# Performance work log

Hardware: AMD Instinct MI355X
Metric: run time of the kernel (lower is better)

Reference implementation:

```python
import jax, jax.numpy as jnp
import numpy as np

N, T = 2000, 8
INFEAT, HID, OUT, H = 32, 16, 32, 4
ALPHA = 0.2
D1 = HID * H   # 64, layer-1 GRU dim (concat heads)
D2 = OUT       # 32, layer-2 GRU dim (mean heads)
NEG = -1e9


def setup_inputs() -> dict:
    key = jax.random.key(0)
    ks = jax.random.split(key, 12)
    xav = lambda k, shape, fi, fo: (jax.random.normal(k, shape, dtype=jnp.float32)
                                    * np.float32(np.sqrt(2.0 / (fi + fo))))
    # sparse-ish binary adjacency with self loops, per timestep
    A = (jax.random.uniform(ks[0], (T, N, N)) < 0.01).astype(jnp.float32)
    A = jnp.maximum(A, jnp.eye(N, dtype=jnp.float32)[None])
    feats = jax.random.normal(ks[1], (T, N, INFEAT), dtype=jnp.float32) * 0.1
    return {
        "A": A,
        "feats": feats,
        "gat1_W": xav(ks[2], (H, INFEAT, HID), INFEAT, HID),
        "gat1_a": xav(ks[3], (H, 2, HID), 2 * HID, 1),
        "gru1_W": xav(ks[4], (3, N, D1, D1), D1, D1),
        "gru1_U": xav(ks[5], (3, N, D1, D1), D1, D1),
        "gru1_b": jnp.zeros((3, N, D1), jnp.float32),
        "q1": xav(ks[6], (N, D1), N, D1),   # GAT_init_features, layer 1
        "gat2_W": xav(ks[7], (H, D1, OUT), D1, OUT),
        "gat2_a": xav(ks[8], (H, 2, OUT), 2 * OUT, 1),
        "gru2_W": xav(ks[9], (3, N, D2, D2), D2, D2),
        "gru2_U": xav(ks[10], (3, N, D2, D2), D2, D2),
        "gru2_b": jnp.zeros((3, N, D2), jnp.float32),
        "q2": xav(ks[11], (N, D2), N, D2),  # GAT_init_features, layer 2
    }


def _gat(x, At, W, a, concat):
    # x: [N,F], At: [N,N], W: [H,F,D], a: [H,2,D]
    h = jnp.einsum('nf,hfd->hnd', x, W)                       # [H,N,D]
    e_src = jnp.einsum('hnd,hd->hn', h, a[:, 0])              # [H,N]
    e_dst = jnp.einsum('hnd,hd->hn', h, a[:, 1])
    e = jax.nn.leaky_relu(e_src[:, :, None] + e_dst[:, None, :], ALPHA)
    e = jnp.where(At[None] > 0, e, NEG)
    att = jax.nn.softmax(e, axis=-1)                          # [H,N,N]
    o = jnp.einsum('hnm,hmd->hnd', att, h)
    if concat:
        return jax.nn.elu(o).transpose(1, 0, 2).reshape(x.shape[0], -1)  # [N,H*D]
    return o.mean(axis=0)                                     # [N,D]


def _gru_step(Q, Z, Wg, Ug, bg):
    # batched per-node mat_GRU_cell: Wg/Ug [3,N,D,D], bg [3,N,D]; gates: update, reset, htilda
    wz = jnp.einsum('gnij,nj->gni', Wg, Z) + bg               # [3,N,D]
    upd = jax.nn.sigmoid(wz[0] + jnp.einsum('nij,nj->ni', Ug[0], Q))
    rst = jax.nn.sigmoid(wz[1] + jnp.einsum('nij,nj->ni', Ug[1], Q))
    hcap = jnp.tanh(wz[2] + jnp.einsum('nij,nj->ni', Ug[2], rst * Q))
    return (1.0 - upd) * Q + upd * hcap


def _grcu_layer(A, feats, q0, W, a, Wg, Ug, bg, concat):
    def step(Q, inp):
        At, xt = inp
        Z = _gat(xt, At, W, a, concat)
        Qn = _gru_step(Q, Z, Wg, Ug, bg)
        return Qn, Qn
    _, seq = jax.lax.scan(step, q0, (A, feats))
    return seq  # [T,N,Dim]


def reference(A, feats, gat1_W, gat1_a, gru1_W, gru1_U, gru1_b, q1,
              gat2_W, gat2_a, gru2_W, gru2_U, gru2_b, q2):
    s1 = _grcu_layer(A, feats, q1, gat1_W, gat1_a, gru1_W, gru1_U, gru1_b, True)
    s2 = _grcu_layer(A, s1, q2, gat2_W, gat2_a, gru2_W, gru2_U, gru2_b, False)
    return s2.reshape(-1, s2.shape[-1])  # torch.cat(out_seq, dim=0) -> [T*N, OUT]
```

## Files before the change

kernel.cpp:

```cpp
#include <hip/hip_runtime.h>
#include <cstdint>
#include <cstddef>

#define NNODES 2000
#define TSTEPS 8
#define NHEADS 4
#define CAP    96
#define NROWS  (TSTEPS * NNODES)

__global__ void k1_csr_gath1(const float* __restrict__ A,
                             int* __restrict__ nbr, int* __restrict__ cnt,
                             const float* __restrict__ feats,
                             const float* __restrict__ W, const float* __restrict__ a,
                             float* __restrict__ hbuf, float* __restrict__ es,
                             float* __restrict__ ed) {
    const int lane = threadIdx.x;
    if (blockIdx.x < NROWS) {
        const int row = blockIdx.x;
        const float4* Ar4 = reinterpret_cast<const float4*>(A + (size_t)row * NNODES);
        int* outp = nbr + (size_t)row * CAP;
        const unsigned long long lmask = (1ull << lane) - 1ull;
        int c = 0;
        for (int j4 = lane; j4 < NNODES / 4; j4 += 64) {
            float4 v = Ar4[j4];
            #pragma unroll
            for (int cc = 0; cc < 4; ++cc) {
                float x = (cc == 0) ? v.x : (cc == 1) ? v.y : (cc == 2) ? v.z : v.w;
                bool p = x > 0.0f;
                unsigned long long m = __ballot(p);
                int off = __popcll(m & lmask);
                if (p && c + off < CAP) outp[c + off] = j4 * 4 + cc;
                c += (int)__popcll(m);
            }
        }
        if (lane == 0) cnt[row] = (c > CAP ? CAP : c);
    } else {
        const int b = blockIdx.x - NROWS;
        const int t = b / NNODES, n = b % NNODES;
        constexpr int F = 32, D = 16;
        const int h = lane / D, d = lane % D;
        const float* xr = feats + (size_t)b * F;
        const float* Wp = W + (size_t)h * F * D + d;
        float acc = 0.f;
        #pragma unroll
        for (int f = 0; f < F; ++f) acc += xr[f] * Wp[f * D];
        hbuf[(((size_t)t * NHEADS + h) * NNODES + n) * D + d] = acc;
        float s0 = acc * a[(h * 2 + 0) * D + d];
        float s1 = acc * a[(h * 2 + 1) * D + d];
        #pragma unroll
        for (int s = D / 2; s > 0; s >>= 1) {
            s0 += __shfl_down(s0, s, D);
            s1 += __shfl_down(s1, s, D);
        }
        if (d == 0) {
            es[((size_t)t * NHEADS + h) * NNODES + n] = s0;
            ed[((size_t)t * NHEADS + h) * NNODES + n] = s1;
        }
    }
}

template<int D, bool CONCAT>
__global__ void gat_attn_all_kernel(const int* __restrict__ nbr, const int* __restrict__ cnt_arr,
                                    const float* __restrict__ hbuf, const float* __restrict__ es,
                                    const float* __restrict__ ed, float* __restrict__ Z) {
    const int b = blockIdx.x;
    const int t = b / NNODES, n = b % NNODES;
    const int tid = threadIdx.x;
    const int h = tid / D, d = tid % D;
    const int cnt = cnt_arr[b];
    const int* idx = nbr + (size_t)b * CAP;
    const float* esb = es + (size_t)t * NHEADS * NNODES;
    const float* edb = ed + (size_t)t * NHEADS * NNODES;
    const float* hb  = hbuf + (size_t)t * NHEADS * NNODES * D;
    __shared__ int mlist[CAP];
    __shared__ float eds[NHEADS][CAP];
    for (int k = tid; k < cnt; k += NHEADS * D) mlist[k] = idx[k];
    __syncthreads();
    for (int k = d; k < cnt; k += D) eds[h][k] = edb[(size_t)h * NNODES + mlist[k]];
    __syncthreads();
    const float esv = esb[(size_t)h * NNODES + n];
    float maxv = -1e30f;
    for (int k = 0; k < cnt; ++k) {
        float v = esv + eds[h][k];
        v = v > 0.f ? v : 0.2f * v;
        maxv = fmaxf(maxv, v);
    }
    float wsum = 0.f, acc = 0.f;
    for (int k = 0; k < cnt; ++k) {
        float v = esv + eds[h][k];
        v = v > 0.f ? v : 0.2f * v;
        float w = __expf(v - maxv);
        wsum += w;
        acc += w * hb[((size_t)h * NNODES + mlist[k]) * D + d];
    }
    float o = acc / wsum;
    if constexpr (CONCAT) {
        float e = o > 0.f ? o : (__expf(o) - 1.0f);
        Z[(size_t)b * (NHEADS * D) + h * D + d] = e;
    } else {
        __shared__ float red[NHEADS][D];
        red[h][d] = o;
        __syncthreads();
        if (h == 0) Z[(size_t)b * D + d] =
            (red[0][d] + red[1][d] + red[2][d] + red[3][d]) * 0.25f;
    }
}

__global__ __launch_bounds__(256, 1)
void wzgru1_gath2_kernel(const float* __restrict__ Wg, const float* __restrict__ Ug,
                         const float* __restrict__ bg, const float* __restrict__ Z,
                         const float* __restrict__ q0,
                         const float* __restrict__ W2, const float* __restrict__ a2,
                         float* __restrict__ h2, float* __restrict__ es2,
                         float* __restrict__ ed2) {
    constexpr int D = 64;
    constexpr int QUADS = 4;
    constexpr int TPB = 256;
    constexpr int F4R = D / 4;
    const int n = blockIdx.x, tid = threadIdx.x;
    const int quad = tid & (QUADS - 1);
    const int row  = tid / QUADS;
    const int cbase = quad * 16;
    __shared__ float Zs[TSTEPS][D];
    __shared__ float Qh[TSTEPS][D];
    __shared__ float Qs[D], rq[D];

    for (int idx = tid; idx < TSTEPS * F4R; idx += TPB) {
        int t = idx / F4R, i4 = idx % F4R;
        reinterpret_cast<float4*>(&Zs[t][0])[i4] =
            reinterpret_cast<const float4*>(Z + ((size_t)t * NNODES + n) * D)[i4];
    }
    if (tid < D) Qs[tid] = q0[(size_t)n * D + tid];
    float bgv[3];
    #pragma unroll
    for (int g = 0; g < 3; ++g) bgv[g] = bg[((size_t)g * NNODES + n) * D + row];

    float wseg[3][16], useg[3][16];
    #pragma unroll
    for (int g = 0; g < 3; ++g) {
        const float4* W4 = reinterpret_cast<const float4*>(
            Wg + ((size_t)g * NNODES + n) * D * D + (size_t)row * D + cbase);
        #pragma unroll
        for (int c = 0; c < 4; ++c) {
            float4 v = W4[c];
            wseg[g][c * 4 + 0] = v.x; wseg[g][c * 4 + 1] = v.y;
            wseg[g][c * 4 + 2] = v.z; wseg[g][c * 4 + 3] = v.w;
        }
    }
    #pragma unroll
    for (int g = 0; g < 3; ++g) {
        const float4* U4 = reinterpret_cast<const float4*>(
            Ug + ((size_t)g * NNODES + n) * D * D + (size_t)row * D + cbase);
        #pragma unroll
        for (int c = 0; c < 4; ++c) {
            float4 v = U4[c];
            useg[g][c * 4 + 0] = v.x; useg[g][c * 4 + 1] = v.y;
            useg[g][c * 4 + 2] = v.z; useg[g][c * 4 + 3] = v.w;
        }
    }
    __syncthreads();

    float wzr[3][TSTEPS];
    #pragma unroll
    for (int t = 0; t < TSTEPS; ++t) {
        float z16[16];
        #pragma unroll
        for (int c = 0; c < 4; ++c) {
            float4 v = reinterpret_cast<const float4*>(&Zs[t][cbase])[c];
            z16[c * 4 + 0] = v.x; z16[c * 4 + 1] = v.y;
            z16[c * 4 + 2] = v.z; z16[c * 4 + 3] = v.w;
        }
        #pragma unroll
        for (int g = 0; g < 3; ++g) {
            float p = 0.f;
            #pragma unroll
            for (int c = 0; c < 16; ++c) p += wseg[g][c] * z16[c];
            p += __shfl_xor(p, 1, 4); p += __shfl_xor(p, 2, 4);
            wzr[g][t] = p + bgv[g];
        }
    }

    #pragma unroll
    for (int t = 0; t < TSTEPS; ++t) {
        float q16[16];
        #pragma unroll
        for (int c = 0; c < 4; ++c) {
            float4 v = reinterpret_cast<const float4*>(&Qs[cbase])[c];
            q16[c * 4 + 0] = v.x; q16[c * 4 + 1] = v.y;
            q16[c * 4 + 2] = v.z; q16[c * 4 + 3] = v.w;
        }
        float p0 = 0.f, p1 = 0.f;
        #pragma unroll
        for (int c = 0; c < 16; ++c) { p0 += useg[0][c] * q16[c]; p1 += useg[1][c] * q16[c]; }
        p0 += __shfl_xor(p0, 1, 4); p0 += __shfl_xor(p0, 2, 4);
        p1 += __shfl_xor(p1, 1, 4); p1 += __shfl_xor(p1, 2, 4);
        const float qrow = Qs[row];
        const float zg = 1.f / (1.f + __expf(-(wzr[0][t] + p0)));
        const float rg = 1.f / (1.f + __expf(-(wzr[1][t] + p1)));
        if (quad == 0) rq[row] = rg * qrow;
        __syncthreads();
        float p2 = 0.f;
        {
            float r16[16];
            #pragma unroll
            for (int c = 0; c < 4; ++c) {
                float4 v = reinterpret_cast<const float4*>(&rq[cbase])[c];
                r16[c * 4 + 0] = v.x; r16[c * 4 + 1] = v.y;
                r16[c * 4 + 2] = v.z; r16[c * 4 + 3] = v.w;
            }
            #pragma unroll
            for (int c = 0; c < 16; ++c) p2 += useg[2][c] * r16[c];
        }
        p2 += __shfl_xor(p2, 1, 4); p2 += __shfl_xor(p2, 2, 4);
        const float hcap = tanhf(wzr[2][t] + p2);
        const float qn = (1.f - zg) * qrow + zg * hcap;
        if (quad == 0) {
            Qs[row] = qn;
            Qh[t][row] = qn;
        }
        __syncthreads();
    }

    const int lane = tid & 63;
    const int hh = tid >> 6;
    const int d2 = lane >> 1;
    const int fh = lane & 1;
    float w2seg[32];
    const float* W2p = W2 + ((size_t)hh * 64 + fh * 32) * 32 + d2;
    #pragma unroll
    for (int j = 0; j < 32; ++j) w2seg[j] = W2p[(size_t)j * 32];
    const float a0 = a2[(hh * 2 + 0) * 32 + d2];
    const float a1 = a2[(hh * 2 + 1) * 32 + d2];
    #pragma unroll
    for (int t = 0; t < TSTEPS; ++t) {
        float p = 0.f;
        #pragma unroll
        for (int j = 0; j < 32; ++j) p += w2seg[j] * Qh[t][fh * 32 + j];
        p += __shfl_xor(p, 1, 64);
        if (fh == 0) h2[(((size_t)t * NHEADS + hh) * NNODES + n) * 32 + d2] = p;
        float e0 = (fh == 0) ? p * a0 : 0.f;
        float e1 = (fh == 0) ? p * a1 : 0.f;
        #pragma unroll
        for (int s = 2; s <= 32; s <<= 1) {
            e0 += __shfl_xor(e0, s, 64);
            e1 += __shfl_xor(e1, s, 64);
        }
        if (lane == 0) {
            es2[((size_t)t * NHEADS + hh) * NNODES + n] = e0;
            ed2[((size_t)t * NHEADS + hh) * NNODES + n] = e1;
        }
    }
}

template<int D>
__global__ __launch_bounds__((D / 16) * D, 1)
void wzgru_kernel(const float* __restrict__ Wg, const float* __restrict__ Ug,
                  const float* __restrict__ bg, const float* __restrict__ Z,
                  const float* __restrict__ q0, float* __restrict__ outp) {
    constexpr int QUADS = D / 16;
    constexpr int TPB = QUADS * D;
    constexpr int F4R = D / 4;
    const int n = blockIdx.x, tid = threadIdx.x;
    const int quad = tid & (QUADS - 1);
    const int row  = tid / QUADS;
    const int cbase = quad * 16;
    __shared__ float Zs[TSTEPS][D];
    __shared__ float Qs[D], rq[D];

    for (int idx = tid; idx < TSTEPS * F4R; idx += TPB) {
        int t = idx / F4R, i4 = idx % F4R;
        reinterpret_cast<float4*>(&Zs[t][0])[i4] =
            reinterpret_cast<const float4*>(Z + ((size_t)t * NNODES + n) * D)[i4];
    }
    if (tid < D) Qs[tid] = q0[(size_t)n * D + tid];
    float bgv[3];
    #pragma unroll
    for (int g = 0; g < 3; ++g) bgv[g] = bg[((size_t)g * NNODES + n) * D + row];

    float wseg[3][16], useg[3][16];
    #pragma unroll
    for (int g = 0; g < 3; ++g) {
        const float4* W4 = reinterpret_cast<const float4*>(
            Wg + ((size_t)g * NNODES + n) * D * D + (size_t)row * D + cbase);
        #pragma unroll
        for (int c = 0; c < 4; ++c) {
            float4 v = W4[c];
            wseg[g][c * 4 + 0] = v.x; wseg[g][c * 4 + 1] = v.y;
            wseg[g][c * 4 + 2] = v.z; wseg[g][c * 4 + 3] = v.w;
        }
    }
    #pragma unroll
    for (int g = 0; g < 3; ++g) {
        const float4* U4 = reinterpret_cast<const float4*>(
            Ug + ((size_t)g * NNODES + n) * D * D + (size_t)row * D + cbase);
        #pragma unroll
        for (int c = 0; c < 4; ++c) {
            float4 v = U4[c];
            useg[g][c * 4 + 0] = v.x; useg[g][c * 4 + 1] = v.y;
            useg[g][c * 4 + 2] = v.z; useg[g][c * 4 + 3] = v.w;
        }
    }
    __syncthreads();

    float wzr[3][TSTEPS];
    #pragma unroll
    for (int t = 0; t < TSTEPS; ++t) {
        float z16[16];
        #pragma unroll
        for (int c = 0; c < 4; ++c) {
            float4 v = reinterpret_cast<const float4*>(&Zs[t][cbase])[c];
            z16[c * 4 + 0] = v.x; z16[c * 4 + 1] = v.y;
            z16[c * 4 + 2] = v.z; z16[c * 4 + 3] = v.w;
        }
        #pragma unroll
        for (int g = 0; g < 3; ++g) {
            float p = 0.f;
            #pragma unroll
            for (int c = 0; c < 16; ++c) p += wseg[g][c] * z16[c];
            if constexpr (QUADS == 4) { p += __shfl_xor(p, 1, 4); p += __shfl_xor(p, 2, 4); }
            else                      { p += __shfl_xor(p, 1, 2); }
            wzr[g][t] = p + bgv[g];
        }
    }

    #pragma unroll
    for (int t = 0; t < TSTEPS; ++t) {
        float q16[16];
        #pragma unroll
        for (int c = 0; c < 4; ++c) {
            float4 v = reinterpret_cast<const float4*>(&Qs[cbase])[c];
            q16[c * 4 + 0] = v.x; q16[c * 4 + 1] = v.y;
            q16[c * 4 + 2] = v.z; q16[c * 4 + 3] = v.w;
        }
        float p0 = 0.f, p1 = 0.f;
        #pragma unroll
        for (int c = 0; c < 16; ++c) { p0 += useg[0][c] * q16[c]; p1 += useg[1][c] * q16[c]; }
        if constexpr (QUADS == 4) {
            p0 += __shfl_xor(p0, 1, 4); p0 += __shfl_xor(p0, 2, 4);
            p1 += __shfl_xor(p1, 1, 4); p1 += __shfl_xor(p1, 2, 4);
        } else {
            p0 += __shfl_xor(p0, 1, 2); p1 += __shfl_xor(p1, 1, 2);
        }
        const float qrow = Qs[row];
        const float zg = 1.f / (1.f + __expf(-(wzr[0][t] + p0)));
        const float rg = 1.f / (1.f + __expf(-(wzr[1][t] + p1)));
        if (quad == 0) rq[row] = rg * qrow;
        __syncthreads();
        float p2 = 0.f;
        {
            float r16[16];
            #pragma unroll
            for (int c = 0; c < 4; ++c) {
                float4 v = reinterpret_cast<const float4*>(&rq[cbase])[c];
                r16[c * 4 + 0] = v.x; r16[c * 4 + 1] = v.y;
                r16[c * 4 + 2] = v.z; r16[c * 4 + 3] = v.w;
            }
            #pragma unroll
            for (int c = 0; c < 16; ++c) p2 += useg[2][c] * r16[c];
        }
        if constexpr (QUADS == 4) { p2 += __shfl_xor(p2, 1, 4); p2 += __shfl_xor(p2, 2, 4); }
        else                      { p2 += __shfl_xor(p2, 1, 2); }
        const float hcap = tanhf(wzr[2][t] + p2);
        const float qn = (1.f - zg) * qrow + zg * hcap;
        if (quad == 0) {
            Qs[row] = qn;
            outp[((size_t)t * NNODES + n) * D + row] = qn;
        }
        __syncthreads();
    }
}

extern "C" void kernel_launch(void* const* d_in, const int* in_sizes, int n_in,
                              void* d_out, int out_size, void* d_ws, size_t ws_size,
                              hipStream_t stream) {
    const float* A      = (const float*)d_in[0];
    const float* feats  = (const float*)d_in[1];
    const float* gat1_W = (const float*)d_in[2];
    const float* gat1_a = (const float*)d_in[3];
    const float* gru1_W = (const float*)d_in[4];
    const float* gru1_U = (const float*)d_in[5];
    const float* gru1_b = (const float*)d_in[6];
    const float* q1     = (const float*)d_in[7];
    const float* gat2_W = (const float*)d_in[8];
    const float* gat2_a = (const float*)d_in[9];
    const float* gru2_W = (const float*)d_in[10];
    const float* gru2_U = (const float*)d_in[11];
    const float* gru2_b = (const float*)d_in[12];
    const float* q2     = (const float*)d_in[13];
    float* out = (float*)d_out;

    char* ws = (char*)d_ws;
    int*   nbr  = (int*)ws;    ws += (size_t)NROWS * CAP * 4;
    int*   cnt  = (int*)ws;    ws += (size_t)NROWS * 4;
    float* h1   = (float*)ws;  ws += (size_t)TSTEPS * NHEADS * NNODES * 16 * 4;
    float* es1  = (float*)ws;  ws += (size_t)TSTEPS * NHEADS * NNODES * 4;
    float* ed1  = (float*)ws;  ws += (size_t)TSTEPS * NHEADS * NNODES * 4;
    float* Z1   = (float*)ws;  ws += (size_t)TSTEPS * NNODES * 64 * 4;
    float* h2   = (float*)ws;  ws += (size_t)TSTEPS * NHEADS * NNODES * 32 * 4;
    float* es2  = (float*)ws;  ws += (size_t)TSTEPS * NHEADS * NNODES * 4;
    float* ed2  = (float*)ws;  ws += (size_t)TSTEPS * NHEADS * NNODES * 4;
    float* Z2   = (float*)ws;  ws += (size_t)TSTEPS * NNODES * 32 * 4;

    k1_csr_gath1<<<2 * NROWS, 64, 0, stream>>>(A, nbr, cnt, feats, gat1_W, gat1_a,
                                               h1, es1, ed1);
    gat_attn_all_kernel<16, true><<<NROWS, 64, 0, stream>>>(nbr, cnt, h1, es1, ed1, Z1);
    wzgru1_gath2_kernel<<<NNODES, 256, 0, stream>>>(gru1_W, gru1_U, gru1_b, Z1, q1,
                                                    gat2_W, gat2_a, h2, es2, ed2);
    gat_attn_all_kernel<32, false><<<NROWS, 128, 0, stream>>>(nbr, cnt, h2, es2, ed2, Z2);
    wzgru_kernel<32><<<NNODES, 64, 0, stream>>>(gru2_W, gru2_U, gru2_b, Z2, q2, out);
}
```

Baseline: 166.3 us.

## Split GRU input projection into separate per-gate kernel before recurrent step

Moves the W·Z input projections for all timesteps out of the fused GRU kernels into a new kernel launched with one block per gate per node, writing results to a workspace buffer. The recurrent kernels then only load U weights and the precomputed wz values, which cuts their register footprint and per-block load latency. The price is an extra round trip of the wz intermediates through global memory and one more launch per layer. The GAT-2 projection also now reads the hidden state from shared memory as float4 vectors.

```diff
diff --git a/kernel.cpp b/kernel.cpp
--- a/kernel.cpp
+++ b/kernel.cpp
@@ -106,47 +106,72 @@
     }
 }
 
-__global__ __launch_bounds__(256, 1)
-void wzgru1_gath2_kernel(const float* __restrict__ Wg, const float* __restrict__ Ug,
-                         const float* __restrict__ bg, const float* __restrict__ Z,
-                         const float* __restrict__ q0,
-                         const float* __restrict__ W2, const float* __restrict__ a2,
-                         float* __restrict__ h2, float* __restrict__ es2,
-                         float* __restrict__ ed2) {
-    constexpr int D = 64;
-    constexpr int QUADS = 4;
-    constexpr int TPB = 256;
+template<int D>
+__global__ __launch_bounds__((D / 16) * D, 1)
+void wz_all_kernel(const float* __restrict__ Wg, const float* __restrict__ bg,
+                   const float* __restrict__ Z, float* __restrict__ wz) {
+    constexpr int QUADS = D / 16;
+    constexpr int TPB = QUADS * D;
     constexpr int F4R = D / 4;
-    const int n = blockIdx.x, tid = threadIdx.x;
+    const int g = blockIdx.x / NNODES;
+    const int n = blockIdx.x % NNODES;
+    const int tid = threadIdx.x;
     const int quad = tid & (QUADS - 1);
     const int row  = tid / QUADS;
     const int cbase = quad * 16;
     __shared__ float Zs[TSTEPS][D];
-    __shared__ float Qh[TSTEPS][D];
-    __shared__ float Qs[D], rq[D];
-
+
+    float wseg[16];
+    {
+        const float4* W4 = reinterpret_cast<const float4*>(
+            Wg + ((size_t)g * NNODES + n) * D * D + (size_t)row * D + cbase);
+        #pragma unroll
+        for (int c = 0; c < 4; ++c) {
+            float4 v = W4[c];
+            wseg[c * 4 + 0] = v.x; wseg[c * 4 + 1] = v.y;
+            wseg[c * 4 + 2] = v.z; wseg[c * 4 + 3] = v.w;
+        }
+    }
+    const float bgv = bg[((size_t)g * NNODES + n) * D + row];
     for (int idx = tid; idx < TSTEPS * F4R; idx += TPB) {
         int t = idx / F4R, i4 = idx % F4R;
         reinterpret_cast<float4*>(&Zs[t][0])[i4] =
             reinterpret_cast<const float4*>(Z + ((size_t)t * NNODES + n) * D)[i4];
     }
-    if (tid < D) Qs[tid] = q0[(size_t)n * D + tid];
-    float bgv[3];
-    #pragma unroll
-    for (int g = 0; g < 3; ++g) bgv[g] = bg[((size_t)g * NNODES + n) * D + row];
-
-    float wseg[3][16], useg[3][16];
-    #pragma unroll
-    for (int g = 0; g < 3; ++g) {
-        const float4* W4 = reinterpret_cast<const float4*>(
-            Wg + ((size_t)g * NNODES + n) * D * D + (size_t)row * D + cbase);
-        #pragma unroll
-        for (int c = 0; c < 4; ++c) {
-            float4 v = W4[c];
-            wseg[g][c * 4 + 0] = v.x; wseg[g][c * 4 + 1] = v.y;
-            wseg[g][c * 4 + 2] = v.z; wseg[g][c * 4 + 3] = v.w;
-        }
-    }
+    __syncthreads();
+    #pragma unroll
+    for (int t = 0; t < TSTEPS; ++t) {
+        float z16[16];
+        #pragma unroll
+        for (int c = 0; c < 4; ++c) {
+            float4 v = reinterpret_cast<const float4*>(&Zs[t][cbase])[c];
+            z16[c * 4 + 0] = v.x; z16[c * 4 + 1] = v.y;
+            z16[c * 4 + 2] = v.z; z16[c * 4 + 3] = v.w;
+        }
+        float p = 0.f;
+        #pragma unroll
+        for (int c = 0; c < 16; ++c) p += wseg[c] * z16[c];
+        if constexpr (QUADS == 4) { p += __shfl_xor(p, 1, 4); p += __shfl_xor(p, 2, 4); }
+        else                      { p += __shfl_xor(p, 1, 2); }
+        if (quad == 0)
+            wz[(((size_t)n * 3 + g) * TSTEPS + t) * D + row] = p + bgv;
+    }
+}
+
+__global__ __launch_bounds__(256, 1)
+void gru1_gath2_kernel(const float* __restrict__ Ug, const float* __restrict__ wzg,
+                       const float* __restrict__ q0,
+                       const float* __restrict__ W2, const float* __restrict__ a2,
+                       float* __restrict__ h2, float* __restrict__ es2,
+                       float* __restrict__ ed2) {
+    constexpr int D = 64;
+    const int n = blockIdx.x, tid = threadIdx.x;
+    const int quad = tid & 3;
+    const int row  = tid >> 2;
+    const int cbase = quad * 16;
+    __shared__ float Qs[D], rq[D], Qh[TSTEPS][D];
+
+    float useg[3][16];
     #pragma unroll
     for (int g = 0; g < 3; ++g) {
         const float4* U4 = reinterpret_cast<const float4*>(
@@ -158,27 +183,21 @@
             useg[g][c * 4 + 2] = v.z; useg[g][c * 4 + 3] = v.w;
         }
     }
+    float wzr[3][TSTEPS];
+    #pragma unroll
+    for (int g = 0; g < 3; ++g)
+        #pragma unroll
+        for (int t = 0; t < TSTEPS; ++t)
+            wzr[g][t] = wzg[(((size_t)n * 3 + g) * TSTEPS + t) * D + row];
+    #pragma unroll
+    for (int g = 0; g < 3; ++g) {
+        #pragma unroll
+        for (int c = 0; c < 16; ++c) asm volatile("" : "+v"(useg[g][c]));
+        #pragma unroll
+        for (int t = 0; t < TSTEPS; ++t) asm volatile("" : "+v"(wzr[g][t]));
+    }
+    if (tid < D) Qs[tid] = q0[(size_t)n * D + tid];
     __syncthreads();
-
-    float wzr[3][TSTEPS];
-    #pragma unroll
-    for (int t = 0; t < TSTEPS; ++t) {
-        float z16[16];
-        #pragma unroll
-        for (int c = 0; c < 4; ++c) {
-            float4 v = reinterpret_cast<const float4*>(&Zs[t][cbase])[c];
-            z16[c * 4 + 0] = v.x; z16[c * 4 + 1] = v.y;
-            z16[c * 4 + 2] = v.z; z16[c * 4 + 3] = v.w;
-        }
-        #pragma unroll
-        for (int g = 0; g < 3; ++g) {
-            float p = 0.f;
-            #pragma unroll
-            for (int c = 0; c < 16; ++c) p += wseg[g][c] * z16[c];
-            p += __shfl_xor(p, 1, 4); p += __shfl_xor(p, 2, 4);
-            wzr[g][t] = p + bgv[g];
-        }
-    }
 
     #pragma unroll
     for (int t = 0; t < TSTEPS; ++t) {
@@ -233,9 +252,16 @@
     const float a1 = a2[(hh * 2 + 1) * 32 + d2];
     #pragma unroll
     for (int t = 0; t < TSTEPS; ++t) {
+        float q32[32];
+        #pragma unroll
+        for (int c = 0; c < 8; ++c) {
+            float4 v = reinterpret_cast<const float4*>(&Qh[t][fh * 32])[c];
+            q32[c * 4 + 0] = v.x; q32[c * 4 + 1] = v.y;
+            q32[c * 4 + 2] = v.z; q32[c * 4 + 3] = v.w;
+        }
         float p = 0.f;
         #pragma unroll
-        for (int j = 0; j < 32; ++j) p += w2seg[j] * Qh[t][fh * 32 + j];
+        for (int j = 0; j < 32; ++j) p += w2seg[j] * q32[j];
         p += __shfl_xor(p, 1, 64);
         if (fh == 0) h2[(((size_t)t * NHEADS + hh) * NNODES + n) * 32 + d2] = p;
         float e0 = (fh == 0) ? p * a0 : 0.f;
@@ -252,43 +278,17 @@
     }
 }
 
-template<int D>
-__global__ __launch_bounds__((D / 16) * D, 1)
-void wzgru_kernel(const float* __restrict__ Wg, const float* __restrict__ Ug,
-                  const float* __restrict__ bg, const float* __restrict__ Z,
-                  const float* __restrict__ q0, float* __restrict__ outp) {
-    constexpr int QUADS = D / 16;
-    constexpr int TPB = QUADS * D;
-    constexpr int F4R = D / 4;
+__global__ __launch_bounds__(64, 1)
+void gru2_kernel(const float* __restrict__ Ug, const float* __restrict__ wzg,
+                 const float* __restrict__ q0, float* __restrict__ outp) {
+    constexpr int D = 32;
     const int n = blockIdx.x, tid = threadIdx.x;
-    const int quad = tid & (QUADS - 1);
-    const int row  = tid / QUADS;
+    const int quad = tid & 1;
+    const int row  = tid >> 1;
     const int cbase = quad * 16;
-    __shared__ float Zs[TSTEPS][D];
     __shared__ float Qs[D], rq[D];
 
-    for (int idx = tid; idx < TSTEPS * F4R; idx += TPB) {
-        int t = idx / F4R, i4 = idx % F4R;
-        reinterpret_cast<float4*>(&Zs[t][0])[i4] =
-            reinterpret_cast<const float4*>(Z + ((size_t)t * NNODES + n) * D)[i4];
-    }
-    if (tid < D) Qs[tid] = q0[(size_t)n * D + tid];
-    float bgv[3];
-    #pragma unroll
-    for (int g = 0; g < 3; ++g) bgv[g] = bg[((size_t)g * NNODES + n) * D + row];
-
-    float wseg[3][16], useg[3][16];
-    #pragma unroll
-    for (int g = 0; g < 3; ++g) {
-        const float4* W4 = reinterpret_cast<const float4*>(
-            Wg + ((size_t)g * NNODES + n) * D * D + (size_t)row * D + cbase);
-        #pragma unroll
-        for (int c = 0; c < 4; ++c) {
-            float4 v = W4[c];
-            wseg[g][c * 4 + 0] = v.x; wseg[g][c * 4 + 1] = v.y;
-            wseg[g][c * 4 + 2] = v.z; wseg[g][c * 4 + 3] = v.w;
-        }
-    }
+    float useg[3][16];
     #pragma unroll
     for (int g = 0; g < 3; ++g) {
         const float4* U4 = reinterpret_cast<const float4*>(
@@ -300,28 +300,21 @@
             useg[g][c * 4 + 2] = v.z; useg[g][c * 4 + 3] = v.w;
         }
     }
+    float wzr[3][TSTEPS];
+    #pragma unroll
+    for (int g = 0; g < 3; ++g)
+        #pragma unroll
+        for (int t = 0; t < TSTEPS; ++t)
+            wzr[g][t] = wzg[(((size_t)n * 3 + g) * TSTEPS + t) * D + row];
+    #pragma unroll
+    for (int g = 0; g < 3; ++g) {
+        #pragma unroll
+        for (int c = 0; c < 16; ++c) asm volatile("" : "+v"(useg[g][c]));
+        #pragma unroll
+        for (int t = 0; t < TSTEPS; ++t) asm volatile("" : "+v"(wzr[g][t]));
+    }
+    if (tid < D) Qs[tid] = q0[(size_t)n * D + tid];
     __syncthreads();
-
-    float wzr[3][TSTEPS];
-    #pragma unroll
-    for (int t = 0; t < TSTEPS; ++t) {
-        float z16[16];
-        #pragma unroll
-        for (int c = 0; c < 4; ++c) {
-            float4 v = reinterpret_cast<const float4*>(&Zs[t][cbase])[c];
-            z16[c * 4 + 0] = v.x; z16[c * 4 + 1] = v.y;
-            z16[c * 4 + 2] = v.z; z16[c * 4 + 3] = v.w;
-        }
-        #pragma unroll
-        for (int g = 0; g < 3; ++g) {
-            float p = 0.f;
-            #pragma unroll
-            for (int c = 0; c < 16; ++c) p += wseg[g][c] * z16[c];
-            if constexpr (QUADS == 4) { p += __shfl_xor(p, 1, 4); p += __shfl_xor(p, 2, 4); }
-            else                      { p += __shfl_xor(p, 1, 2); }
-            wzr[g][t] = p + bgv[g];
-        }
-    }
 
     #pragma unroll
     for (int t = 0; t < TSTEPS; ++t) {
@@ -335,12 +328,8 @@
         float p0 = 0.f, p1 = 0.f;
         #pragma unroll
         for (int c = 0; c < 16; ++c) { p0 += useg[0][c] * q16[c]; p1 += useg[1][c] * q16[c]; }
-        if constexpr (QUADS == 4) {
-            p0 += __shfl_xor(p0, 1, 4); p0 += __shfl_xor(p0, 2, 4);
-            p1 += __shfl_xor(p1, 1, 4); p1 += __shfl_xor(p1, 2, 4);
-        } else {
-            p0 += __shfl_xor(p0, 1, 2); p1 += __shfl_xor(p1, 1, 2);
-        }
+        p0 += __shfl_xor(p0, 1, 2);
+        p1 += __shfl_xor(p1, 1, 2);
         const float qrow = Qs[row];
         const float zg = 1.f / (1.f + __expf(-(wzr[0][t] + p0)));
         const float rg = 1.f / (1.f + __expf(-(wzr[1][t] + p1)));
@@ -358,8 +347,7 @@
             #pragma unroll
             for (int c = 0; c < 16; ++c) p2 += useg[2][c] * r16[c];
         }
-        if constexpr (QUADS == 4) { p2 += __shfl_xor(p2, 1, 4); p2 += __shfl_xor(p2, 2, 4); }
-        else                      { p2 += __shfl_xor(p2, 1, 2); }
+        p2 += __shfl_xor(p2, 1, 2);
         const float hcap = tanhf(wzr[2][t] + p2);
         const float qn = (1.f - zg) * qrow + zg * hcap;
         if (quad == 0) {
@@ -396,16 +384,20 @@
     float* es1  = (float*)ws;  ws += (size_t)TSTEPS * NHEADS * NNODES * 4;
     float* ed1  = (float*)ws;  ws += (size_t)TSTEPS * NHEADS * NNODES * 4;
     float* Z1   = (float*)ws;  ws += (size_t)TSTEPS * NNODES * 64 * 4;
+    float* wz1  = (float*)ws;  ws += (size_t)NNODES * 3 * TSTEPS * 64 * 4;
     float* h2   = (float*)ws;  ws += (size_t)TSTEPS * NHEADS * NNODES * 32 * 4;
     float* es2  = (float*)ws;  ws += (size_t)TSTEPS * NHEADS * NNODES * 4;
     float* ed2  = (float*)ws;  ws += (size_t)TSTEPS * NHEADS * NNODES * 4;
     float* Z2   = (float*)ws;  ws += (size_t)TSTEPS * NNODES * 32 * 4;
+    float* wz2  = (float*)ws;  ws += (size_t)NNODES * 3 * TSTEPS * 32 * 4;
 
     k1_csr_gath1<<<2 * NROWS, 64, 0, stream>>>(A, nbr, cnt, feats, gat1_W, gat1_a,
                                                h1, es1, ed1);
     gat_attn_all_kernel<16, true><<<NROWS, 64, 0, stream>>>(nbr, cnt, h1, es1, ed1, Z1);
-    wzgru1_gath2_kernel<<<NNODES, 256, 0, stream>>>(gru1_W, gru1_U, gru1_b, Z1, q1,
-                                                    gat2_W, gat2_a, h2, es2, ed2);
+    wz_all_kernel<64><<<3 * NNODES, 256, 0, stream>>>(gru1_W, gru1_b, Z1, wz1);
+    gru1_gath2_kernel<<<NNODES, 256, 0, stream>>>(gru1_U, wz1, q1,
+                                                  gat2_W, gat2_a, h2, es2, ed2);
     gat_attn_all_kernel<32, false><<<NROWS, 128, 0, stream>>>(nbr, cnt, h2, es2, ed2, Z2);
-    wzgru_kernel<32><<<NNODES, 64, 0, stream>>>(gru2_W, gru2_U, gru2_b, Z2, q2, out);
-}
+    wz_all_kernel<32><<<3 * NNODES, 64, 0, stream>>>(gru2_W, gru2_b, Z2, wz2);
+    gru2_kernel<<<NNODES, 64, 0, stream>>>(gru2_U, wz2, q2, out);
+}
```

New measurement: 175.2 us. 5.3% more time.

## Fuse GAT attention into per-node GRU kernels, eliminating Z buffers and launches

Applied to the files above, without the earlier changes.

Moves the neighbor-softmax attention for each layer into the per-node GRU kernels. Each block now computes Z for all timesteps of its node directly into shared memory, so the Z1/Z2 round trips and two kernel launches go away. Weight loads are issued before the attention gather and pinned with asm barriers to overlap memory latency. Layer 2 also changes from 64 to 128 threads using 8-column segments. The cost is that attention now runs inside only 2000 blocks instead of 16000, which lowers parallelism for that phase.

```diff
diff --git a/kernel.cpp b/kernel.cpp
--- a/kernel.cpp
+++ b/kernel.cpp
@@ -59,83 +59,26 @@
     }
 }
 
-template<int D, bool CONCAT>
-__global__ void gat_attn_all_kernel(const int* __restrict__ nbr, const int* __restrict__ cnt_arr,
-                                    const float* __restrict__ hbuf, const float* __restrict__ es,
-                                    const float* __restrict__ ed, float* __restrict__ Z) {
-    const int b = blockIdx.x;
-    const int t = b / NNODES, n = b % NNODES;
-    const int tid = threadIdx.x;
-    const int h = tid / D, d = tid % D;
-    const int cnt = cnt_arr[b];
-    const int* idx = nbr + (size_t)b * CAP;
-    const float* esb = es + (size_t)t * NHEADS * NNODES;
-    const float* edb = ed + (size_t)t * NHEADS * NNODES;
-    const float* hb  = hbuf + (size_t)t * NHEADS * NNODES * D;
-    __shared__ int mlist[CAP];
-    __shared__ float eds[NHEADS][CAP];
-    for (int k = tid; k < cnt; k += NHEADS * D) mlist[k] = idx[k];
-    __syncthreads();
-    for (int k = d; k < cnt; k += D) eds[h][k] = edb[(size_t)h * NNODES + mlist[k]];
-    __syncthreads();
-    const float esv = esb[(size_t)h * NNODES + n];
-    float maxv = -1e30f;
-    for (int k = 0; k < cnt; ++k) {
-        float v = esv + eds[h][k];
-        v = v > 0.f ? v : 0.2f * v;
-        maxv = fmaxf(maxv, v);
-    }
-    float wsum = 0.f, acc = 0.f;
-    for (int k = 0; k < cnt; ++k) {
-        float v = esv + eds[h][k];
-        v = v > 0.f ? v : 0.2f * v;
-        float w = __expf(v - maxv);
-        wsum += w;
-        acc += w * hb[((size_t)h * NNODES + mlist[k]) * D + d];
-    }
-    float o = acc / wsum;
-    if constexpr (CONCAT) {
-        float e = o > 0.f ? o : (__expf(o) - 1.0f);
-        Z[(size_t)b * (NHEADS * D) + h * D + d] = e;
-    } else {
-        __shared__ float red[NHEADS][D];
-        red[h][d] = o;
-        __syncthreads();
-        if (h == 0) Z[(size_t)b * D + d] =
-            (red[0][d] + red[1][d] + red[2][d] + red[3][d]) * 0.25f;
-    }
-}
-
 __global__ __launch_bounds__(256, 1)
-void wzgru1_gath2_kernel(const float* __restrict__ Wg, const float* __restrict__ Ug,
-                         const float* __restrict__ bg, const float* __restrict__ Z,
-                         const float* __restrict__ q0,
-                         const float* __restrict__ W2, const float* __restrict__ a2,
-                         float* __restrict__ h2, float* __restrict__ es2,
-                         float* __restrict__ ed2) {
+void layer1_kernel(const int* __restrict__ nbr, const int* __restrict__ cnt,
+                   const float* __restrict__ h1, const float* __restrict__ es1,
+                   const float* __restrict__ ed1,
+                   const float* __restrict__ Wg, const float* __restrict__ Ug,
+                   const float* __restrict__ bg, const float* __restrict__ q0,
+                   const float* __restrict__ W2, const float* __restrict__ a2,
+                   float* __restrict__ h2, float* __restrict__ es2,
+                   float* __restrict__ ed2) {
     constexpr int D = 64;
-    constexpr int QUADS = 4;
-    constexpr int TPB = 256;
-    constexpr int F4R = D / 4;
     const int n = blockIdx.x, tid = threadIdx.x;
-    const int quad = tid & (QUADS - 1);
-    const int row  = tid / QUADS;
+    const int quad = tid & 3;
+    const int row  = tid >> 2;
     const int cbase = quad * 16;
+    __shared__ int   mlist[4][CAP];
+    __shared__ float eds[4][NHEADS][CAP];
     __shared__ float Zs[TSTEPS][D];
-    __shared__ float Qh[TSTEPS][D];
-    __shared__ float Qs[D], rq[D];
-
-    for (int idx = tid; idx < TSTEPS * F4R; idx += TPB) {
-        int t = idx / F4R, i4 = idx % F4R;
-        reinterpret_cast<float4*>(&Zs[t][0])[i4] =
-            reinterpret_cast<const float4*>(Z + ((size_t)t * NNODES + n) * D)[i4];
-    }
-    if (tid < D) Qs[tid] = q0[(size_t)n * D + tid];
-    float bgv[3];
-    #pragma unroll
-    for (int g = 0; g < 3; ++g) bgv[g] = bg[((size_t)g * NNODES + n) * D + row];
-
-    float wseg[3][16], useg[3][16];
+    __shared__ float Qs[D], rqv[D], Qh[TSTEPS][D];
+
+    float wseg[3][16];
     #pragma unroll
     for (int g = 0; g < 3; ++g) {
         const float4* W4 = reinterpret_cast<const float4*>(
@@ -147,6 +90,72 @@
             wseg[g][c * 4 + 2] = v.z; wseg[g][c * 4 + 3] = v.w;
         }
     }
+    float bgv[3];
+    #pragma unroll
+    for (int g = 0; g < 3; ++g) bgv[g] = bg[((size_t)g * NNODES + n) * D + row];
+    if (tid < D) Qs[tid] = q0[(size_t)n * D + tid];
+
+    const int w    = tid >> 6;
+    const int lane = tid & 63;
+    const int hh   = lane >> 4;
+    const int dd   = lane & 15;
+    #pragma unroll
+    for (int half = 0; half < 2; ++half) {
+        const int t = half * 4 + w;
+        const int b = t * NNODES + n;
+        const int cntb = cnt[b];
+        __syncthreads();
+        for (int k = lane; k < cntb; k += 64) mlist[w][k] = nbr[(size_t)b * CAP + k];
+        __syncthreads();
+        for (int k = dd; k < cntb; k += 16)
+            eds[w][hh][k] = ed1[((size_t)t * NHEADS + hh) * NNODES + mlist[w][k]];
+        __syncthreads();
+        const float esv = es1[((size_t)t * NHEADS + hh) * NNODES + n];
+        float maxv = -1e30f;
+        for (int k = 0; k < cntb; ++k) {
+            float v = esv + eds[w][hh][k];
+            v = v > 0.f ? v : 0.2f * v;
+            maxv = fmaxf(maxv, v);
+        }
+        const float* hb = h1 + (size_t)t * NHEADS * NNODES * 16;
+        float wsum = 0.f, acc = 0.f;
+        for (int k = 0; k < cntb; ++k) {
+            float v = esv + eds[w][hh][k];
+            v = v > 0.f ? v : 0.2f * v;
+            float wgt = __expf(v - maxv);
+            wsum += wgt;
+            acc += wgt * hb[((size_t)hh * NNODES + mlist[w][k]) * 16 + dd];
+        }
+        float o = acc / wsum;
+        Zs[t][hh * 16 + dd] = o > 0.f ? o : (__expf(o) - 1.0f);
+    }
+    #pragma unroll
+    for (int g = 0; g < 3; ++g)
+        #pragma unroll
+        for (int c = 0; c < 16; ++c) asm volatile("" : "+v"(wseg[g][c]));
+    __syncthreads();
+
+    float wzr[3][TSTEPS];
+    #pragma unroll
+    for (int t = 0; t < TSTEPS; ++t) {
+        float z16[16];
+        #pragma unroll
+        for (int c = 0; c < 4; ++c) {
+            float4 v = reinterpret_cast<const float4*>(&Zs[t][cbase])[c];
+            z16[c * 4 + 0] = v.x; z16[c * 4 + 1] = v.y;
+            z16[c * 4 + 2] = v.z; z16[c * 4 + 3] = v.w;
+        }
+        #pragma unroll
+        for (int g = 0; g < 3; ++g) {
+            float p = 0.f;
+            #pragma unroll
+            for (int c = 0; c < 16; ++c) p += wseg[g][c] * z16[c];
+            p += __shfl_xor(p, 1, 4); p += __shfl_xor(p, 2, 4);
+            wzr[g][t] = p + bgv[g];
+        }
+    }
+
+    float useg[3][16];
     #pragma unroll
     for (int g = 0; g < 3; ++g) {
         const float4* U4 = reinterpret_cast<const float4*>(
@@ -158,27 +167,10 @@
             useg[g][c * 4 + 2] = v.z; useg[g][c * 4 + 3] = v.w;
         }
     }
-    __syncthreads();
-
-    float wzr[3][TSTEPS];
-    #pragma unroll
-    for (int t = 0; t < TSTEPS; ++t) {
-        float z16[16];
-        #pragma unroll
-        for (int c = 0; c < 4; ++c) {
-            float4 v = reinterpret_cast<const float4*>(&Zs[t][cbase])[c];
-            z16[c * 4 + 0] = v.x; z16[c * 4 + 1] = v.y;
-            z16[c * 4 + 2] = v.z; z16[c * 4 + 3] = v.w;
-        }
-        #pragma unroll
-        for (int g = 0; g < 3; ++g) {
-            float p = 0.f;
-            #pragma unroll
-            for (int c = 0; c < 16; ++c) p += wseg[g][c] * z16[c];
-            p += __shfl_xor(p, 1, 4); p += __shfl_xor(p, 2, 4);
-            wzr[g][t] = p + bgv[g];
-        }
-    }
+    #pragma unroll
+    for (int g = 0; g < 3; ++g)
+        #pragma unroll
+        for (int c = 0; c < 16; ++c) asm volatile("" : "+v"(useg[g][c]));
 
     #pragma unroll
     for (int t = 0; t < TSTEPS; ++t) {
@@ -197,14 +189,14 @@
         const float qrow = Qs[row];
         const float zg = 1.f / (1.f + __expf(-(wzr[0][t] + p0)));
         const float rg = 1.f / (1.f + __expf(-(wzr[1][t] + p1)));
-        if (quad == 0) rq[row] = rg * qrow;
+        if (quad == 0) rqv[row] = rg * qrow;
         __syncthreads();
         float p2 = 0.f;
         {
             float r16[16];
             #pragma unroll
             for (int c = 0; c < 4; ++c) {
-                float4 v = reinterpret_cast<const float4*>(&rq[cbase])[c];
+                float4 v = reinterpret_cast<const float4*>(&rqv[cbase])[c];
                 r16[c * 4 + 0] = v.x; r16[c * 4 + 1] = v.y;
                 r16[c * 4 + 2] = v.z; r16[c * 4 + 3] = v.w;
             }
@@ -221,23 +213,28 @@
         __syncthreads();
     }
 
-    const int lane = tid & 63;
-    const int hh = tid >> 6;
     const int d2 = lane >> 1;
     const int fh = lane & 1;
     float w2seg[32];
-    const float* W2p = W2 + ((size_t)hh * 64 + fh * 32) * 32 + d2;
+    const float* W2p = W2 + ((size_t)w * 64 + fh * 32) * 32 + d2;
     #pragma unroll
     for (int j = 0; j < 32; ++j) w2seg[j] = W2p[(size_t)j * 32];
-    const float a0 = a2[(hh * 2 + 0) * 32 + d2];
-    const float a1 = a2[(hh * 2 + 1) * 32 + d2];
-    #pragma unroll
-    for (int t = 0; t < TSTEPS; ++t) {
+    const float a0 = a2[(w * 2 + 0) * 32 + d2];
+    const float a1 = a2[(w * 2 + 1) * 32 + d2];
+    #pragma unroll
+    for (int t = 0; t < TSTEPS; ++t) {
+        float q32[32];
+        #pragma unroll
+        for (int c = 0; c < 8; ++c) {
+            float4 v = reinterpret_cast<const float4*>(&Qh[t][fh * 32])[c];
+            q32[c * 4 + 0] = v.x; q32[c * 4 + 1] = v.y;
+            q32[c * 4 + 2] = v.z; q32[c * 4 + 3] = v.w;
+        }
         float p = 0.f;
         #pragma unroll
-        for (int j = 0; j < 32; ++j) p += w2seg[j] * Qh[t][fh * 32 + j];
+        for (int j = 0; j < 32; ++j) p += w2seg[j] * q32[j];
         p += __shfl_xor(p, 1, 64);
-        if (fh == 0) h2[(((size_t)t * NHEADS + hh) * NNODES + n) * 32 + d2] = p;
+        if (fh == 0) h2[(((size_t)t * NHEADS + w) * NNODES + n) * 32 + d2] = p;
         float e0 = (fh == 0) ? p * a0 : 0.f;
         float e1 = (fh == 0) ? p * a1 : 0.f;
         #pragma unroll
@@ -246,120 +243,154 @@
             e1 += __shfl_xor(e1, s, 64);
         }
         if (lane == 0) {
-            es2[((size_t)t * NHEADS + hh) * NNODES + n] = e0;
-            ed2[((size_t)t * NHEADS + hh) * NNODES + n] = e1;
+            es2[((size_t)t * NHEADS + w) * NNODES + n] = e0;
+            ed2[((size_t)t * NHEADS + w) * NNODES + n] = e1;
         }
     }
 }
 
-template<int D>
-__global__ __launch_bounds__((D / 16) * D, 1)
-void wzgru_kernel(const float* __restrict__ Wg, const float* __restrict__ Ug,
-                  const float* __restrict__ bg, const float* __restrict__ Z,
-                  const float* __restrict__ q0, float* __restrict__ outp) {
-    constexpr int QUADS = D / 16;
-    constexpr int TPB = QUADS * D;
-    constexpr int F4R = D / 4;
+__global__ __launch_bounds__(128, 1)
+void layer2_kernel(const int* __restrict__ nbr, const int* __restrict__ cnt,
+                   const float* __restrict__ h2, const float* __restrict__ es2,
+                   const float* __restrict__ ed2,
+                   const float* __restrict__ Wg, const float* __restrict__ Ug,
+                   const float* __restrict__ bg, const float* __restrict__ q0,
+                   float* __restrict__ outp) {
+    constexpr int D = 32;
     const int n = blockIdx.x, tid = threadIdx.x;
-    const int quad = tid & (QUADS - 1);
-    const int row  = tid / QUADS;
-    const int cbase = quad * 16;
+    const int quad = tid & 3;
+    const int row  = tid >> 2;
+    const int cbase = quad * 8;
+    __shared__ int   mlist[CAP];
+    __shared__ float eds[NHEADS][CAP];
+    __shared__ float red[NHEADS][D];
     __shared__ float Zs[TSTEPS][D];
-    __shared__ float Qs[D], rq[D];
-
-    for (int idx = tid; idx < TSTEPS * F4R; idx += TPB) {
-        int t = idx / F4R, i4 = idx % F4R;
-        reinterpret_cast<float4*>(&Zs[t][0])[i4] =
-            reinterpret_cast<const float4*>(Z + ((size_t)t * NNODES + n) * D)[i4];
-    }
-    if (tid < D) Qs[tid] = q0[(size_t)n * D + tid];
-    float bgv[3];
-    #pragma unroll
-    for (int g = 0; g < 3; ++g) bgv[g] = bg[((size_t)g * NNODES + n) * D + row];
-
-    float wseg[3][16], useg[3][16];
+    __shared__ float Qs[D], rqv[D];
+
+    float wseg[3][8];
     #pragma unroll
     for (int g = 0; g < 3; ++g) {
         const float4* W4 = reinterpret_cast<const float4*>(
             Wg + ((size_t)g * NNODES + n) * D * D + (size_t)row * D + cbase);
         #pragma unroll
-        for (int c = 0; c < 4; ++c) {
+        for (int c = 0; c < 2; ++c) {
             float4 v = W4[c];
             wseg[g][c * 4 + 0] = v.x; wseg[g][c * 4 + 1] = v.y;
             wseg[g][c * 4 + 2] = v.z; wseg[g][c * 4 + 3] = v.w;
         }
     }
+    float bgv[3];
+    #pragma unroll
+    for (int g = 0; g < 3; ++g) bgv[g] = bg[((size_t)g * NNODES + n) * D + row];
+    if (tid < D) Qs[tid] = q0[(size_t)n * D + tid];
+
+    const int hh = tid >> 5;
+    const int dd = tid & 31;
+    for (int t = 0; t < TSTEPS; ++t) {
+        const int b = t * NNODES + n;
+        const int cntb = cnt[b];
+        __syncthreads();
+        for (int k = tid; k < cntb; k += 128) mlist[k] = nbr[(size_t)b * CAP + k];
+        __syncthreads();
+        for (int k = dd; k < cntb; k += 32)
+            eds[hh][k] = ed2[((size_t)t * NHEADS + hh) * NNODES + mlist[k]];
+        __syncthreads();
+        const float esv = es2[((size_t)t * NHEADS + hh) * NNODES + n];
+        float maxv = -1e30f;
+        for (int k = 0; k < cntb; ++k) {
+            float v = esv + eds[hh][k];
+            v = v > 0.f ? v : 0.2f * v;
+            maxv = fmaxf(maxv, v);
+        }
+        const float* hb = h2 + (size_t)t * NHEADS * NNODES * 32;
+        float wsum = 0.f, acc = 0.f;
+        for (int k = 0; k < cntb; ++k) {
+            float v = esv + eds[hh][k];
+            v = v > 0.f ? v : 0.2f * v;
+            float wgt = __expf(v - maxv);
+            wsum += wgt;
+            acc += wgt * hb[((size_t)hh * NNODES + mlist[k]) * 32 + dd];
+        }
+        red[hh][dd] = acc / wsum;
+        __syncthreads();
+        if (hh == 0)
+            Zs[t][dd] = (red[0][dd] + red[1][dd] + red[2][dd] + red[3][dd]) * 0.25f;
+    }
+    #pragma unroll
+    for (int g = 0; g < 3; ++g)
+        #pragma unroll
+        for (int c = 0; c < 8; ++c) asm volatile("" : "+v"(wseg[g][c]));
+    __syncthreads();
+
+    float wzr[3][TSTEPS];
+    #pragma unroll
+    for (int t = 0; t < TSTEPS; ++t) {
+        float z8[8];
+        #pragma unroll
+        for (int c = 0; c < 2; ++c) {
+            float4 v = reinterpret_cast<const float4*>(&Zs[t][cbase])[c];
+            z8[c * 4 + 0] = v.x; z8[c * 4 + 1] = v.y;
+            z8[c * 4 + 2] = v.z; z8[c * 4 + 3] = v.w;
+        }
+        #pragma unroll
+        for (int g = 0; g < 3; ++g) {
+            float p = 0.f;
+            #pragma unroll
+            for (int c = 0; c < 8; ++c) p += wseg[g][c] * z8[c];
+            p += __shfl_xor(p, 1, 4); p += __shfl_xor(p, 2, 4);
+            wzr[g][t] = p + bgv[g];
+        }
+    }
+
+    float useg[3][8];
     #pragma unroll
     for (int g = 0; g < 3; ++g) {
         const float4* U4 = reinterpret_cast<const float4*>(
             Ug + ((size_t)g * NNODES + n) * D * D + (size_t)row * D + cbase);
         #pragma unroll
-        for (int c = 0; c < 4; ++c) {
+        for (int c = 0; c < 2; ++c) {
             float4 v = U4[c];
             useg[g][c * 4 + 0] = v.x; useg[g][c * 4 + 1] = v.y;
             useg[g][c * 4 + 2] = v.z; useg[g][c * 4 + 3] = v.w;
         }
     }
-    __syncthreads();
-
-    float wzr[3][TSTEPS];
-    #pragma unroll
-    for (int t = 0; t < TSTEPS; ++t) {
-        float z16[16];
-        #pragma unroll
-        for (int c = 0; c < 4; ++c) {
-            float4 v = reinterpret_cast<const float4*>(&Zs[t][cbase])[c];
-            z16[c * 4 + 0] = v.x; z16[c * 4 + 1] = v.y;
-            z16[c * 4 + 2] = v.z; z16[c * 4 + 3] = v.w;
-        }
-        #pragma unroll
-        for (int g = 0; g < 3; ++g) {
-            float p = 0.f;
-            #pragma unroll
-            for (int c = 0; c < 16; ++c) p += wseg[g][c] * z16[c];
-            if constexpr (QUADS == 4) { p += __shfl_xor(p, 1, 4); p += __shfl_xor(p, 2, 4); }
-            else                      { p += __shfl_xor(p, 1, 2); }
-            wzr[g][t] = p + bgv[g];
-        }
-    }
-
-    #pragma unroll
-    for (int t = 0; t < TSTEPS; ++t) {
-        float q16[16];
-        #pragma unroll
-        for (int c = 0; c < 4; ++c) {
+    #pragma unroll
+    for (int g = 0; g < 3; ++g)
+        #pragma unroll
+        for (int c = 0; c < 8; ++c) asm volatile("" : "+v"(useg[g][c]));
+
+    #pragma unroll
+    for (int t = 0; t < TSTEPS; ++t) {
+        float q8[8];
+        #pragma unroll
+        for (int c = 0; c < 2; ++c) {
             float4 v = reinterpret_cast<const float4*>(&Qs[cbase])[c];
-            q16[c * 4 + 0] = v.x; q16[c * 4 + 1] = v.y;
-            q16[c * 4 + 2] = v.z; q16[c * 4 + 3] = v.w;
+            q8[c * 4 + 0] = v.x; q8[c * 4 + 1] = v.y;
+            q8[c * 4 + 2] = v.z; q8[c * 4 + 3] = v.w;
         }
         float p0 = 0.f, p1 = 0.f;
         #pragma unroll
-        for (int c = 0; c < 16; ++c) { p0 += useg[0][c] * q16[c]; p1 += useg[1][c] * q16[c]; }
-        if constexpr (QUADS == 4) {
-            p0 += __shfl_xor(p0, 1, 4); p0 += __shfl_xor(p0, 2, 4);
-            p1 += __shfl_xor(p1, 1, 4); p1 += __shfl_xor(p1, 2, 4);
-        } else {
-            p0 += __shfl_xor(p0, 1, 2); p1 += __shfl_xor(p1, 1, 2);
-        }
+        for (int c = 0; c < 8; ++c) { p0 += useg[0][c] * q8[c]; p1 += useg[1][c] * q8[c]; }
+        p0 += __shfl_xor(p0, 1, 4); p0 += __shfl_xor(p0, 2, 4);
+        p1 += __shfl_xor(p1, 1, 4); p1 += __shfl_xor(p1, 2, 4);
         const float qrow = Qs[row];
         const float zg = 1.f / (1.f + __expf(-(wzr[0][t] + p0)));
         const float rg = 1.f / (1.f + __expf(-(wzr[1][t] + p1)));
-        if (quad == 0) rq[row] = rg * qrow;
+        if (quad == 0) rqv[row] = rg * qrow;
         __syncthreads();
         float p2 = 0.f;
         {
-            float r16[16];
-            #pragma unroll
-            for (int c = 0; c < 4; ++c) {
-                float4 v = reinterpret_cast<const float4*>(&rq[cbase])[c];
-                r16[c * 4 + 0] = v.x; r16[c * 4 + 1] = v.y;
-                r16[c * 4 + 2] = v.z; r16[c * 4 + 3] = v.w;
+            float r8[8];
+            #pragma unroll
+            for (int c = 0; c < 2; ++c) {
+                float4 v = reinterpret_cast<const float4*>(&rqv[cbase])[c];
+                r8[c * 4 + 0] = v.x; r8[c * 4 + 1] = v.y;
+                r8[c * 4 + 2] = v.z; r8[c * 4 + 3] = v.w;
             }
             #pragma unroll
-            for (int c = 0; c < 16; ++c) p2 += useg[2][c] * r16[c];
-        }
-        if constexpr (QUADS == 4) { p2 += __shfl_xor(p2, 1, 4); p2 += __shfl_xor(p2, 2, 4); }
-        else                      { p2 += __shfl_xor(p2, 1, 2); }
+            for (int c = 0; c < 8; ++c) p2 += useg[2][c] * r8[c];
+        }
+        p2 += __shfl_xor(p2, 1, 4); p2 += __shfl_xor(p2, 2, 4);
         const float hcap = tanhf(wzr[2][t] + p2);
         const float qn = (1.f - zg) * qrow + zg * hcap;
         if (quad == 0) {
@@ -395,17 +426,15 @@
     float* h1   = (float*)ws;  ws += (size_t)TSTEPS * NHEADS * NNODES * 16 * 4;
     float* es1  = (float*)ws;  ws += (size_t)TSTEPS * NHEADS * NNODES * 4;
     float* ed1  = (float*)ws;  ws += (size_t)TSTEPS * NHEADS * NNODES * 4;
-    float* Z1   = (float*)ws;  ws += (size_t)TSTEPS * NNODES * 64 * 4;
     float* h2   = (float*)ws;  ws += (size_t)TSTEPS * NHEADS * NNODES * 32 * 4;
     float* es2  = (float*)ws;  ws += (size_t)TSTEPS * NHEADS * NNODES * 4;
     float* ed2  = (float*)ws;  ws += (size_t)TSTEPS * NHEADS * NNODES * 4;
-    float* Z2   = (float*)ws;  ws += (size_t)TSTEPS * NNODES * 32 * 4;
 
     k1_csr_gath1<<<2 * NROWS, 64, 0, stream>>>(A, nbr, cnt, feats, gat1_W, gat1_a,
                                                h1, es1, ed1);
-    gat_attn_all_kernel<16, true><<<NROWS, 64, 0, stream>>>(nbr, cnt, h1, es1, ed1, Z1);
-    wzgru1_gath2_kernel<<<NNODES, 256, 0, stream>>>(gru1_W, gru1_U, gru1_b, Z1, q1,
-                                                    gat2_W, gat2_a, h2, es2, ed2);
-    gat_attn_all_kernel<32, false><<<NROWS, 128, 0, stream>>>(nbr, cnt, h2, es2, ed2, Z2);
-    wzgru_kernel<32><<<NNODES, 64, 0, stream>>>(gru2_W, gru2_U, gru2_b, Z2, q2, out);
+    layer1_kernel<<<NNODES, 256, 0, stream>>>(nbr, cnt, h1, es1, ed1,
+                                              gru1_W, gru1_U, gru1_b, q1,
+                                              gat2_W, gat2_a, h2, es2, ed2);
+    layer2_kernel<<<NNODES, 128, 0, stream>>>(nbr, cnt, h2, es2, ed2,
+                                              gru2_W, gru2_U, gru2_b, q2, out);
 }
```

After: 250.1 us. 1.5x slower.
